# Performance work log

Hardware: AMD Instinct MI355X
Metric: run time of the kernel (lower is better)

The kernel has to match this reference:

```python
import jax, jax.numpy as jnp
from jax import lax
import numpy as np

N = 10                      # spline knots
STEP = 1.0 / (N - 1)
B, E, NC, H, W = 64, 2, 8, 256, 256

def _interp_matrix(n, step):
    # natural-cubic-spline second-derivative solve matrix (constant, numpy at trace time)
    mat = 4.0 * np.eye(n - 2)
    np.fill_diagonal(mat[1:, :-1], 1.0)
    np.fill_diagonal(mat[:-1, 1:], 1.0)
    A = 6.0 * np.linalg.inv(mat) / step ** 2
    z = np.zeros(n - 2)
    A = np.vstack([z, A, z])
    Bm = np.zeros([n - 2, n])
    np.fill_diagonal(Bm, 1.0)
    np.fill_diagonal(Bm[:, 1:], -2.0)
    np.fill_diagonal(Bm[:, 2:], 1.0)
    return (A @ Bm).astype(np.float32)

MAT = jnp.asarray(_interp_matrix(N, STEP))  # (N, N)


def setup_inputs() -> dict:
    key = jax.random.key(0)
    ks = iter(jax.random.split(key, 40))
    def w(shape, scale=0.05):
        return jax.random.normal(next(ks), shape, jnp.float32) * scale
    d = {"batch": jax.random.uniform(next(ks), (B, 3, H, W), jnp.float32)}
    chans = [3, NC, 2 * NC, 4 * NC, 8 * NC, 16 * NC]
    for i in range(1, 6):
        d[f"w{i}"] = w((chans[i], chans[i - 1], 3, 3))
        d[f"bias{i}"] = jnp.zeros((chans[i],), jnp.float32)
    for i in range(2, 6):
        c = chans[i]
        d[f"bn{i}_gamma"] = jnp.ones((c,), jnp.float32)
        d[f"bn{i}_beta"] = jnp.zeros((c,), jnp.float32)
        d[f"bn{i}_mean"] = jnp.zeros((c,), jnp.float32)
        d[f"bn{i}_var"] = jnp.ones((c,), jnp.float32)
    d["l1_w"] = w((16 * NC, 16 * NC))
    d["l1_b"] = jnp.zeros((16 * NC,), jnp.float32)
    d["l2_w"] = w((3 * N * E, 16 * NC))
    d["l2_b"] = jnp.zeros((3 * N * E,), jnp.float32)
    return d


def _conv(x, w, b):
    y = lax.conv_general_dilated(x, w, (2, 2), 'VALID',
                                 dimension_numbers=('NCHW', 'OIHW', 'NCHW'))
    return y + b[None, :, None, None]


def _bn(x, g, beta, m, v):
    s = (g * lax.rsqrt(v + 1e-5))
    return (x - m[None, :, None, None]) * s[None, :, None, None] + beta[None, :, None, None]


def _coeffs(yt):
    # yt: (B, E, 3, N) knot values (ys + identity). Returns a,b,c,d each (B,E,3,N-1).
    M = jnp.einsum('ij,becj->beci', MAT, yt)
    h = STEP
    a = (M[..., 1:] - M[..., :-1]) / (6.0 * h)
    b = M[..., :-1] / 2.0
    c = (yt[..., 1:] - yt[..., :-1]) / h - (M[..., 1:] + 2.0 * M[..., :-1]) * (h / 6.0)
    d = yt[..., :-1]
    return a, b, c, d


def _apply(a, b, c, d, xi, xf):
    # a..d: (B,E,3,N-1); xi int (B,E,3,P); xf float broadcastable to (B,E,3,P)
    ga = jnp.take_along_axis(a, xi, axis=-1)
    gb = jnp.take_along_axis(b, xi, axis=-1)
    gc = jnp.take_along_axis(c, xi, axis=-1)
    gd = jnp.take_along_axis(d, xi, axis=-1)
    return ((ga * xf + gb) * xf + gc) * xf + gd


def reference(batch, w1, bias1, w2, bias2, w3, bias3, w4, bias4, w5, bias5,
              bn2_gamma, bn2_beta, bn2_mean, bn2_var,
              bn3_gamma, bn3_beta, bn3_mean, bn3_var,
              bn4_gamma, bn4_beta, bn4_mean, bn4_var,
              bn5_gamma, bn5_beta, bn5_mean, bn5_var,
              l1_w, l1_b, l2_w, l2_b):
    y = jax.nn.relu(_conv(batch, w1, bias1))
    y = _bn(jax.nn.relu(_conv(y, w2, bias2)), bn2_gamma, bn2_beta, bn2_mean, bn2_var)
    y = _bn(jax.nn.relu(_conv(y, w3, bias3)), bn3_gamma, bn3_beta, bn3_mean, bn3_var)
    y = _bn(jax.nn.relu(_conv(y, w4, bias4)), bn4_gamma, bn4_beta, bn4_mean, bn4_var)
    y = _bn(jax.nn.relu(_conv(y, w5, bias5)), bn5_gamma, bn5_beta, bn5_mean, bn5_var)
    feat = jnp.mean(y, axis=(2, 3))                      # AvgPool2d(7) on 7x7 -> (B, 16*NC)
    hh = jax.nn.relu(feat @ l1_w.T + l1_b)
    ys = (hh @ l2_w.T + l2_b).reshape(B, E, 3, N)        # per-expert per-channel knot residuals
    identity = (jnp.arange(N, dtype=jnp.float32) / (N - 1))
    yt = ys + identity                                   # residual curves around identity
    a, b, c, d = _coeffs(yt)                             # each (B,E,3,N-1)

    # per-pixel bucketize + coefficient gather + cubic Horner eval
    P = H * W
    xv = batch.reshape(B, 3, P)
    xi = jnp.clip(jnp.floor(xv / STEP), 0, N - 2).astype(jnp.int32)
    xf = (xv - xi.astype(jnp.float32) * STEP)[:, None, :, :]       # (B,1,3,P)
    idx = jnp.broadcast_to(xi[:, None, :, :], (B, E, 3, P))
    out = _apply(a, b, c, d, idx, xf)                              # (B,E,3,P)
    out = out.reshape(B, E, 3, H, W).transpose(1, 0, 2, 3, 4)      # (E,B,3,H,W)

    # sampled spline curves over 255 uniform values
    vals = jnp.arange(0.0, 1.0, 1.0 / 255, dtype=jnp.float32)      # (255,)
    V = vals.shape[0]
    vi = jnp.clip(jnp.floor(vals / STEP), 0, N - 2).astype(jnp.int32)
    vf = vals - vi.astype(jnp.float32) * STEP
    vidx = jnp.broadcast_to(vi[None, None, None, :], (B, E, 3, V))
    splines = _apply(a, b, c, d, vidx, vf[None, None, None, :])    # (B,E,3,V)
    splines = splines.transpose(1, 0, 2, 3)                        # (E,B,3,V)
    return out, splines
```

## Files before the change

kernel.cpp:

```cpp
#include <hip/hip_runtime.h>
#include <hip/hip_bf16.h>

#define STEP_F (1.0f/9.0f)

typedef float f4 __attribute__((ext_vector_type(4)));

__global__ __launch_bounds__(256) void conv12_k(
    const float* __restrict__ x,
    const float* __restrict__ w1c, const float* __restrict__ b1c,
    const float* __restrict__ w2c, const float* __restrict__ b2c,
    const float* __restrict__ g, const float* __restrict__ be,
    const float* __restrict__ mn, const float* __restrict__ vr,
    float* __restrict__ y2)
{
    __shared__ float y1t[8 * 1188 + 16];
    const int b    = blockIdx.x;
    const int ohg  = blockIdx.y;
    const int tid  = threadIdx.x;
    const int rows = (127 - 8 * ohg) < 9 ? (127 - 8 * ohg) : 9;

    {
        const int owg = tid & 31;
        const int rg  = tid >> 5;
        const float* xb = x + (size_t)b * 3 * 65536;
        for (int r = rg; r < rows; r += 8) {
            const int r1  = 8 * ohg + r;
            const int ih0 = 2 * r1;
            const int iw0 = owg * 8;
            float acc1[8][4];
            #pragma unroll
            for (int c = 0; c < 8; ++c)
                #pragma unroll
                for (int t = 0; t < 4; ++t) acc1[c][t] = 0.0f;

            #pragma unroll
            for (int ci = 0; ci < 3; ++ci) {
                float rr[3][10];
                #pragma unroll
                for (int kh = 0; kh < 3; ++kh) {
                    const float* row = xb + ci * 65536 + (ih0 + kh) * 256;
                    #pragma unroll
                    for (int t = 0; t < 5; ++t) {
                        int c = iw0 + 2 * t; if (c > 254) c = 254;
                        float2 v = *(const float2*)(row + c);
                        rr[kh][2*t] = v.x; rr[kh][2*t+1] = v.y;
                    }
                }
                #pragma unroll
                for (int co = 0; co < 8; ++co) {
                    float wr[9];
                    #pragma unroll
                    for (int k = 0; k < 9; ++k) wr[k] = w1c[(co * 3 + ci) * 9 + k];
                    #pragma unroll
                    for (int t = 0; t < 4; ++t) {
                        float a = acc1[co][t];
                        #pragma unroll
                        for (int kh = 0; kh < 3; ++kh)
                            a = fmaf(rr[kh][2*t+0], wr[kh*3+0],
                                fmaf(rr[kh][2*t+1], wr[kh*3+1],
                                fmaf(rr[kh][2*t+2], wr[kh*3+2], a)));
                        acc1[co][t] = a;
                    }
                }
            }
            #pragma unroll
            for (int co = 0; co < 8; ++co) {
                float bs = b1c[co];
                f4 o;
                o[0] = fmaxf(acc1[co][0] + bs, 0.0f);
                o[1] = fmaxf(acc1[co][1] + bs, 0.0f);
                o[2] = fmaxf(acc1[co][2] + bs, 0.0f);
                o[3] = fmaxf(acc1[co][3] + bs, 0.0f);
                *(f4*)&y1t[co * 1188 + r * 132 + owg * 4] = o;
            }
        }
    }
    __syncthreads();

    {
        const int lane = tid & 63;
        const int wv   = __builtin_amdgcn_readfirstlane(tid >> 6);
        const int ow   = lane;
        const int co0  = wv * 4;

        float acc[4][4];
        #pragma unroll
        for (int c = 0; c < 4; ++c)
            #pragma unroll
            for (int j = 0; j < 4; ++j) acc[c][j] = 0.0f;

        #pragma unroll 2
        for (int ci = 0; ci < 8; ++ci) {
            float wr[4][9];
            #pragma unroll
            for (int c = 0; c < 4; ++c) {
                const int wb = __builtin_amdgcn_readfirstlane(((co0 + c) * 8 + ci) * 9);
                #pragma unroll
                for (int k = 0; k < 9; ++k) wr[c][k] = w2c[wb + k];
            }
            const float* lci = y1t + ci * 1188;
            #pragma unroll
            for (int r = 0; r < 9; ++r) {
                float2 x01 = *(const float2*)&lci[r * 132 + 2 * ow];
                float  x2  = lci[r * 132 + 2 * ow + 2];
                #pragma unroll
                for (int kh = 0; kh < 3; ++kh) {
                    const int jj = r - kh;
                    if (jj >= 0 && (jj & 1) == 0 && (jj >> 1) < 4) {
                        const int j = jj >> 1;
                        #pragma unroll
                        for (int c = 0; c < 4; ++c)
                            acc[c][j] = fmaf(x01.x, wr[c][kh*3+0],
                                        fmaf(x01.y, wr[c][kh*3+1],
                                        fmaf(x2,    wr[c][kh*3+2], acc[c][j])));
                    }
                }
            }
        }

        if (ow < 63) {
            #pragma unroll
            for (int c = 0; c < 4; ++c) {
                const int co = co0 + c;
                const float bs = b2c[co];
                const float s  = g[co] / sqrtf(vr[co] + 1e-5f);
                const float sh = be[co] - mn[co] * s;
                #pragma unroll
                for (int j = 0; j < 4; ++j) {
                    int oh = 4 * ohg + j;
                    if (oh < 63)
                        y2[(((size_t)b * 16 + co) * 63 + oh) * 64 + ow] =
                            fmaxf(acc[c][j] + bs, 0.0f) * s + sh;
                }
            }
        }
    }
}

__global__ __launch_bounds__(256) void conv3c_k(
    const float* __restrict__ x,
    const float* __restrict__ w, const float* __restrict__ bias,
    const float* __restrict__ g, const float* __restrict__ be,
    const float* __restrict__ mn, const float* __restrict__ vr,
    float* __restrict__ y)
{
    const int b   = blockIdx.x;
    const int ohg = blockIdx.y;
    const int coh = blockIdx.z;
    const int lane = threadIdx.x & 63;
    const int wv   = __builtin_amdgcn_readfirstlane(threadIdx.x >> 6);
    const int ow   = lane & 31;
    const int ohl  = lane >> 5;
    const int co0  = coh * 8 + wv * 2;
    const int ihb  = ohg * 8 + ohl * 4;

    float acc[2][2];
    #pragma unroll
    for (int c = 0; c < 2; ++c) { acc[c][0] = 0.0f; acc[c][1] = 0.0f; }

    #pragma unroll 2
    for (int ci = 0; ci < 16; ++ci) {
        const float* gp = x + (((size_t)b * 16 + ci) * 63) * 64 + 2 * ow;
        f4 rv[5];
        #pragma unroll
        for (int r = 0; r < 5; ++r) {
            int ih = ihb + r; ih = ih > 62 ? 62 : ih;
            rv[r] = *(const f4*)(gp + ih * 64);
        }
        float wr[2][9];
        #pragma unroll
        for (int c = 0; c < 2; ++c) {
            const int wb = __builtin_amdgcn_readfirstlane(((co0 + c) * 16 + ci) * 9);
            #pragma unroll
            for (int k = 0; k < 9; ++k) wr[c][k] = w[wb + k];
        }
        #pragma unroll
        for (int j = 0; j < 2; ++j)
            #pragma unroll
            for (int kh = 0; kh < 3; ++kh) {
                const f4 v = rv[2*j + kh];
                #pragma unroll
                for (int c = 0; c < 2; ++c)
                    acc[c][j] = fmaf(v[0], wr[c][kh*3+0],
                                fmaf(v[1], wr[c][kh*3+1],
                                fmaf(v[2], wr[c][kh*3+2], acc[c][j])));
            }
    }

    if (ow < 31) {
        #pragma unroll
        for (int c = 0; c < 2; ++c) {
            const int co = co0 + c;
            const float bs = bias[co];
            const float s  = g[co] / sqrtf(vr[co] + 1e-5f);
            const float sh = be[co] - mn[co] * s;
            #pragma unroll
            for (int j = 0; j < 2; ++j) {
                int oh = ohg * 4 + ohl * 2 + j;
                if (oh < 31)
                    y[(((size_t)b * 32 + co) * 31 + oh) * 32 + ow] =
                        fmaxf(acc[c][j] + bs, 0.0f) * s + sh;
            }
        }
    }
}

__global__ __launch_bounds__(256) void conv4c_k(
    const float* __restrict__ x,
    const float* __restrict__ w, const float* __restrict__ bias,
    const float* __restrict__ g, const float* __restrict__ be,
    const float* __restrict__ mn, const float* __restrict__ vr,
    float* __restrict__ y)
{
    const int b   = blockIdx.x;
    const int ohg = blockIdx.y;
    const int cog = blockIdx.z;
    const int lane = threadIdx.x & 63;
    const int wv   = __builtin_amdgcn_readfirstlane(threadIdx.x >> 6);
    const int ow   = lane & 15;
    const int ohl  = lane >> 4;
    const int oh   = ohg * 4 + ohl;
    const int co0  = cog * 8 + wv * 2;
    const int ihb  = 2 * oh;

    float acc[2];
    acc[0] = 0.0f; acc[1] = 0.0f;

    #pragma unroll 4
    for (int ci = 0; ci < 32; ++ci) {
        const float* gp = x + (((size_t)b * 32 + ci) * 31) * 32 + 2 * ow;
        f4 rv[3];
        #pragma unroll
        for (int r = 0; r < 3; ++r) {
            int ih = ihb + r; ih = ih > 30 ? 30 : ih;
            rv[r] = *(const f4*)(gp + ih * 32);
        }
        float wr[2][9];
        #pragma unroll
        for (int c = 0; c < 2; ++c) {
            const int wb = __builtin_amdgcn_readfirstlane(((co0 + c) * 32 + ci) * 9);
            #pragma unroll
            for (int k = 0; k < 9; ++k) wr[c][k] = w[wb + k];
        }
        #pragma unroll
        for (int kh = 0; kh < 3; ++kh) {
            const f4 v = rv[kh];
            #pragma unroll
            for (int c = 0; c < 2; ++c)
                acc[c] = fmaf(v[0], wr[c][kh*3+0],
                         fmaf(v[1], wr[c][kh*3+1],
                         fmaf(v[2], wr[c][kh*3+2], acc[c])));
        }
    }

    if (ow < 15 && oh < 15) {
        #pragma unroll
        for (int c = 0; c < 2; ++c) {
            const int co = co0 + c;
            const float bs = bias[co];
            const float s  = g[co] / sqrtf(vr[co] + 1e-5f);
            const float sh = be[co] - mn[co] * s;
            y[(((size_t)b * 64 + co) * 15 + oh) * 16 + ow] =
                fmaxf(acc[c] + bs, 0.0f) * s + sh;
        }
    }
}

__global__ __launch_bounds__(256) void conv5m3_k(
    const float* __restrict__ x,
    const float* __restrict__ w, const float* __restrict__ bias,
    const float* __restrict__ g, const float* __restrict__ be,
    const float* __restrict__ mn, const float* __restrict__ vr,
    float* __restrict__ feat)
{
    __shared__ float red[4 * 325 + 16];
    const int b    = blockIdx.x;
    const int co0  = blockIdx.y * 4;
    const int tid  = threadIdx.x;
    const int wv   = __builtin_amdgcn_readfirstlane(tid >> 6);
    const int lane = tid & 63;
    const int pr = lane >> 3, pc = lane & 7;

    float acc[4];
    #pragma unroll
    for (int c = 0; c < 4; ++c) acc[c] = 0.0f;

    #pragma unroll 4
    for (int i = 0; i < 16; ++i) {
        const int ci = wv * 16 + i;
        const float* gp = x + (((size_t)b * 64 + ci) * 15) * 16 + 2 * pc;
        f4 rv[3];
        #pragma unroll
        for (int r = 0; r < 3; ++r) {
            int ih = 2 * pr + r; ih = ih > 14 ? 14 : ih;
            rv[r] = *(const f4*)(gp + ih * 16);
        }
        float wr[4][9];
        #pragma unroll
        for (int c = 0; c < 4; ++c) {
            const int wb = __builtin_amdgcn_readfirstlane(((co0 + c) * 64 + ci) * 9);
            #pragma unroll
            for (int k = 0; k < 9; ++k) wr[c][k] = w[wb + k];
        }
        #pragma unroll
        for (int kh = 0; kh < 3; ++kh) {
            const f4 v = rv[kh];
            #pragma unroll
            for (int c = 0; c < 4; ++c)
                acc[c] = fmaf(v[0], wr[c][kh*3+0],
                         fmaf(v[1], wr[c][kh*3+1],
                         fmaf(v[2], wr[c][kh*3+2], acc[c])));
        }
    }

    #pragma unroll
    for (int c = 0; c < 4; ++c) red[wv * 325 + lane * 5 + c] = acc[c];
    __syncthreads();
    if (wv == 0) {
        const bool act = (pr < 7) && (pc < 7);
        #pragma unroll
        for (int c = 0; c < 4; ++c) {
            float v = red[lane*5+c] + red[325+lane*5+c]
                    + red[650+lane*5+c] + red[975+lane*5+c];
            const int co = co0 + c;
            const float s = g[co] / sqrtf(vr[co] + 1e-5f);
            v = fmaxf(v + bias[co], 0.0f) * s + (be[co] - mn[co] * s);
            v = act ? v : 0.0f;
            #pragma unroll
            for (int off = 32; off; off >>= 1) v += __shfl_xor(v, off, 64);
            if (lane == 0) feat[(size_t)b * 128 + co] = v * (1.0f / 49.0f);
        }
    }
}

__global__ __launch_bounds__(256) void tail_k(
    const float* __restrict__ featg, const float* __restrict__ l1w,
    const float* __restrict__ l1b, const float* __restrict__ l2w,
    const float* __restrict__ l2b, float* __restrict__ coef,
    float* __restrict__ spl)
{
    __shared__ float feat[128];
    __shared__ float hh[128];
    __shared__ float ysv[64];
    __shared__ float cfl[216];
    const int b = blockIdx.x, t = threadIdx.x;

    if (t < 128) feat[t] = featg[(size_t)b * 128 + t];
    __syncthreads();
    if (t < 128) {
        const float4* wp = (const float4*)(l1w + (size_t)t * 128);
        float s = l1b[t];
        #pragma unroll 8
        for (int k = 0; k < 32; ++k) {
            float4 v = wp[k];
            s += v.x*feat[4*k] + v.y*feat[4*k+1] + v.z*feat[4*k+2] + v.w*feat[4*k+3];
        }
        hh[t] = fmaxf(s, 0.0f);
    }
    __syncthreads();
    if (t < 60) {
        const float4* wp = (const float4*)(l2w + (size_t)t * 128);
        float s = l2b[t];
        #pragma unroll 8
        for (int k = 0; k < 32; ++k) {
            float4 v = wp[k];
            s += v.x*hh[4*k] + v.y*hh[4*k+1] + v.z*hh[4*k+2] + v.w*hh[4*k+3];
        }
        ysv[t] = s;
    }
    __syncthreads();
    if (t < 6) {
        const float h = STEP_F;
        float yt[10];
        #pragma unroll
        for (int n = 0; n < 10; ++n) yt[n] = ysv[t * 10 + n] + (float)n * h;
        float r[8];
        const float k6h2 = 6.0f / (h * h);
        #pragma unroll
        for (int i = 0; i < 8; ++i) r[i] = k6h2 * (yt[i] - 2.0f * yt[i+1] + yt[i+2]);
        float cp[8], dp[8];
        cp[0] = 0.25f; dp[0] = r[0] * 0.25f;
        #pragma unroll
        for (int i = 1; i < 8; ++i) {
            float m = 4.0f - cp[i-1];
            cp[i] = 1.0f / m;
            dp[i] = (r[i] - dp[i-1]) / m;
        }
        float M[10];
        M[0] = 0.0f; M[9] = 0.0f; M[8] = dp[7];
        #pragma unroll
        for (int i = 6; i >= 0; --i) M[i+1] = dp[i] - cp[i] * M[i+2];
        float* cg = coef + ((size_t)b * 6 + t) * 36;
        #pragma unroll
        for (int i = 0; i < 9; ++i) {
            float ca = (M[i+1] - M[i]) / (6.0f * h);
            float cb = M[i] * 0.5f;
            float cc = (yt[i+1] - yt[i]) / h - (M[i+1] + 2.0f * M[i]) * (h / 6.0f);
            float cd = yt[i];
            cfl[t*36 + i]      = ca;  cg[i]      = ca;
            cfl[t*36 + 9 + i]  = cb;  cg[9 + i]  = cb;
            cfl[t*36 + 18 + i] = cc;  cg[18 + i] = cc;
            cfl[t*36 + 27 + i] = cd;  cg[27 + i] = cd;
        }
    }
    __syncthreads();
    for (int i = t; i < 1530; i += 256) {
        int v = i % 255, ec = i / 255;
        float val = (float)v * (1.0f / 255.0f);
        int vi = (int)floorf(val / STEP_F);
        vi = vi < 0 ? 0 : (vi > 8 ? 8 : vi);
        float vf = val - (float)vi * STEP_F;
        const float* c = cfl + ec * 36;
        int e = ec / 3, ch = ec % 3;
        spl[(((size_t)e * 64 + b) * 3 + ch) * 255 + v] =
            ((c[vi]*vf + c[9+vi])*vf + c[18+vi])*vf + c[27+vi];
    }
}

__global__ __launch_bounds__(256) void apply2_k(const float* __restrict__ batch,
                                                const float* __restrict__ coef,
                                                float* __restrict__ out)
{
    int bc = blockIdx.y;
    int b = bc / 3, ch = bc % 3;
    int lane = threadIdx.x & 63;
    int j = lane < 9 ? lane : 8;
    const float* c0p = coef + ((size_t)(b * 6 + 0 + ch)) * 36;
    const float* c1p = coef + ((size_t)(b * 6 + 3 + ch)) * 36;
    float A0 = c0p[j], B0 = c0p[9 + j], C0 = c0p[18 + j], D0 = c0p[27 + j];
    float A1 = c1p[j], B1 = c1p[9 + j], C1 = c1p[18 + j], D1 = c1p[27 + j];

    const int P = 65536;
    size_t base = ((size_t)b * 3 + ch) * P;
    int p0 = (blockIdx.x * blockDim.x + threadIdx.x) * 4;

    float4 xv = *(const float4*)(batch + base + p0);
    float xs[4] = {xv.x, xv.y, xv.z, xv.w};
    float r0[4], r1[4];
    #pragma unroll
    for (int k = 0; k < 4; ++k) {
        float x = xs[k];
        int xi = (int)floorf(x / STEP_F);
        xi = xi < 0 ? 0 : (xi > 8 ? 8 : xi);
        float xf = x - (float)xi * STEP_F;
        int bidx = xi << 2;
        float ga0 = __int_as_float(__builtin_amdgcn_ds_bpermute(bidx, __float_as_int(A0)));
        float gb0 = __int_as_float(__builtin_amdgcn_ds_bpermute(bidx, __float_as_int(B0)));
        float gc0 = __int_as_float(__builtin_amdgcn_ds_bpermute(bidx, __float_as_int(C0)));
        float gd0 = __int_as_float(__builtin_amdgcn_ds_bpermute(bidx, __float_as_int(D0)));
        float ga1 = __int_as_float(__builtin_amdgcn_ds_bpermute(bidx, __float_as_int(A1)));
        float gb1 = __int_as_float(__builtin_amdgcn_ds_bpermute(bidx, __float_as_int(B1)));
        float gc1 = __int_as_float(__builtin_amdgcn_ds_bpermute(bidx, __float_as_int(C1)));
        float gd1 = __int_as_float(__builtin_amdgcn_ds_bpermute(bidx, __float_as_int(D1)));
        r0[k] = fmaf(fmaf(fmaf(ga0, xf, gb0), xf, gc0), xf, gd0);
        r1[k] = fmaf(fmaf(fmaf(ga1, xf, gb1), xf, gc1), xf, gd1);
    }
    float4 o0 = {r0[0], r0[1], r0[2], r0[3]};
    float4 o1 = {r1[0], r1[1], r1[2], r1[3]};
    size_t off0 = (((size_t)0 * 64 + b) * 3 + ch) * P + p0;
    size_t off1 = (((size_t)1 * 64 + b) * 3 + ch) * P + p0;
    *(float4*)(out + off0) = o0;
    *(float4*)(out + off1) = o1;
}

extern "C" void kernel_launch(void* const* d_in, const int* in_sizes, int n_in,
                              void* d_out, int out_size, void* d_ws, size_t ws_size,
                              hipStream_t stream) {
    const float* batch = (const float*)d_in[0];
    const float* w1 = (const float*)d_in[1];  const float* b1 = (const float*)d_in[2];
    const float* w2 = (const float*)d_in[3];  const float* b2 = (const float*)d_in[4];
    const float* w3 = (const float*)d_in[5];  const float* b3 = (const float*)d_in[6];
    const float* w4 = (const float*)d_in[7];  const float* b4 = (const float*)d_in[8];
    const float* w5 = (const float*)d_in[9];  const float* b5 = (const float*)d_in[10];
    const float* bn2g = (const float*)d_in[11]; const float* bn2b = (const float*)d_in[12];
    const float* bn2m = (const float*)d_in[13]; const float* bn2v = (const float*)d_in[14];
    const float* bn3g = (const float*)d_in[15]; const float* bn3b = (const float*)d_in[16];
    const float* bn3m = (const float*)d_in[17]; const float* bn3v = (const float*)d_in[18];
    const float* bn4g = (const float*)d_in[19]; const float* bn4b = (const float*)d_in[20];
    const float* bn4m = (const float*)d_in[21]; const float* bn4v = (const float*)d_in[22];
    const float* bn5g = (const float*)d_in[23]; const float* bn5b = (const float*)d_in[24];
    const float* bn5m = (const float*)d_in[25]; const float* bn5v = (const float*)d_in[26];
    const float* l1w = (const float*)d_in[27]; const float* l1b = (const float*)d_in[28];
    const float* l2w = (const float*)d_in[29]; const float* l2b = (const float*)d_in[30];

    float* outp = (float*)d_out;
    float* y2 = outp;
    float* y3 = y2 + 4128768;
    float* y4 = y3 + 2031616;

    float* coef  = (float*)d_ws;
    float* featw = coef + 13824;

    const int TPB = 256;
    conv12_k<<<dim3(64, 16), TPB, 0, stream>>>(batch, w1, b1, w2, b2,
                                               bn2g, bn2b, bn2m, bn2v, y2);
    conv3c_k<<<dim3(64, 8, 4), TPB, 0, stream>>>(y2, w3, b3, bn3g, bn3b, bn3m, bn3v, y3);
    conv4c_k<<<dim3(64, 4, 8), TPB, 0, stream>>>(y3, w4, b4, bn4g, bn4b, bn4m, bn4v, y4);
    conv5m3_k<<<dim3(64, 32), TPB, 0, stream>>>(y4, w5, b5, bn5g, bn5b, bn5m, bn5v, featw);
    tail_k<<<64, TPB, 0, stream>>>(featw, l1w, l1b, l2w, l2b, coef, outp + 25165824);
    {
        dim3 grid(64, 192);
        apply2_k<<<grid, TPB, 0, stream>>>(batch, coef, outp);
    }
}
```

Before: 145.5 us.

## Widen conv channel tiles, stage conv5 weights in LDS, fuse tail into apply

conv3 and conv4 now compute four output channels per wave instead of two, halving their grids so each input load feeds more FMAs. conv5 computes eight channels per block and stages the block's weight slice in shared memory instead of issuing scalar global loads. The separate tail kernel (MLP plus spline coefficients) is folded into the apply kernel, so each block recomputes the MLP for its (batch, channel) and then loops over eight pixel chunks; this drops one launch and the coefficient round-trip through workspace. In exchange the MLP is computed redundantly in every block, there is less parallelism in the convs, and register pressure rises.

```diff
diff --git a/kernel.cpp b/kernel.cpp
--- a/kernel.cpp
+++ b/kernel.cpp
@@ -137,7 +137,7 @@
     }
 }
 
-__global__ __launch_bounds__(256) void conv3c_k(
+__global__ __launch_bounds__(256) void conv3_k(
     const float* __restrict__ x,
     const float* __restrict__ w, const float* __restrict__ bias,
     const float* __restrict__ g, const float* __restrict__ be,
@@ -151,14 +151,14 @@
     const int wv   = __builtin_amdgcn_readfirstlane(threadIdx.x >> 6);
     const int ow   = lane & 31;
     const int ohl  = lane >> 5;
-    const int co0  = coh * 8 + wv * 2;
+    const int co0  = coh * 16 + wv * 4;
     const int ihb  = ohg * 8 + ohl * 4;
 
-    float acc[2][2];
+    float acc[4][2];
     #pragma unroll
-    for (int c = 0; c < 2; ++c) { acc[c][0] = 0.0f; acc[c][1] = 0.0f; }
-
-    #pragma unroll 2
+    for (int c = 0; c < 4; ++c) { acc[c][0] = 0.0f; acc[c][1] = 0.0f; }
+
+    #pragma unroll 4
     for (int ci = 0; ci < 16; ++ci) {
         const float* gp = x + (((size_t)b * 16 + ci) * 63) * 64 + 2 * ow;
         f4 rv[5];
@@ -167,9 +167,9 @@
             int ih = ihb + r; ih = ih > 62 ? 62 : ih;
             rv[r] = *(const f4*)(gp + ih * 64);
         }
-        float wr[2][9];
-        #pragma unroll
-        for (int c = 0; c < 2; ++c) {
+        float wr[4][9];
+        #pragma unroll
+        for (int c = 0; c < 4; ++c) {
             const int wb = __builtin_amdgcn_readfirstlane(((co0 + c) * 16 + ci) * 9);
             #pragma unroll
             for (int k = 0; k < 9; ++k) wr[c][k] = w[wb + k];
@@ -180,7 +180,7 @@
             for (int kh = 0; kh < 3; ++kh) {
                 const f4 v = rv[2*j + kh];
                 #pragma unroll
-                for (int c = 0; c < 2; ++c)
+                for (int c = 0; c < 4; ++c)
                     acc[c][j] = fmaf(v[0], wr[c][kh*3+0],
                                 fmaf(v[1], wr[c][kh*3+1],
                                 fmaf(v[2], wr[c][kh*3+2], acc[c][j])));
@@ -189,7 +189,7 @@
 
     if (ow < 31) {
         #pragma unroll
-        for (int c = 0; c < 2; ++c) {
+        for (int c = 0; c < 4; ++c) {
             const int co = co0 + c;
             const float bs = bias[co];
             const float s  = g[co] / sqrtf(vr[co] + 1e-5f);
@@ -205,7 +205,7 @@
     }
 }
 
-__global__ __launch_bounds__(256) void conv4c_k(
+__global__ __launch_bounds__(256) void conv4_k(
     const float* __restrict__ x,
     const float* __restrict__ w, const float* __restrict__ bias,
     const float* __restrict__ g, const float* __restrict__ be,
@@ -220,11 +220,12 @@
     const int ow   = lane & 15;
     const int ohl  = lane >> 4;
     const int oh   = ohg * 4 + ohl;
-    const int co0  = cog * 8 + wv * 2;
+    const int co0  = cog * 16 + wv * 4;
     const int ihb  = 2 * oh;
 
-    float acc[2];
-    acc[0] = 0.0f; acc[1] = 0.0f;
+    float acc[4];
+    #pragma unroll
+    for (int c = 0; c < 4; ++c) acc[c] = 0.0f;
 
     #pragma unroll 4
     for (int ci = 0; ci < 32; ++ci) {
@@ -235,9 +236,9 @@
             int ih = ihb + r; ih = ih > 30 ? 30 : ih;
             rv[r] = *(const f4*)(gp + ih * 32);
         }
-        float wr[2][9];
-        #pragma unroll
-        for (int c = 0; c < 2; ++c) {
+        float wr[4][9];
+        #pragma unroll
+        for (int c = 0; c < 4; ++c) {
             const int wb = __builtin_amdgcn_readfirstlane(((co0 + c) * 32 + ci) * 9);
             #pragma unroll
             for (int k = 0; k < 9; ++k) wr[c][k] = w[wb + k];
@@ -246,7 +247,7 @@
         for (int kh = 0; kh < 3; ++kh) {
             const f4 v = rv[kh];
             #pragma unroll
-            for (int c = 0; c < 2; ++c)
+            for (int c = 0; c < 4; ++c)
                 acc[c] = fmaf(v[0], wr[c][kh*3+0],
                          fmaf(v[1], wr[c][kh*3+1],
                          fmaf(v[2], wr[c][kh*3+2], acc[c])));
@@ -255,7 +256,7 @@
 
     if (ow < 15 && oh < 15) {
         #pragma unroll
-        for (int c = 0; c < 2; ++c) {
+        for (int c = 0; c < 4; ++c) {
             const int co = co0 + c;
             const float bs = bias[co];
             const float s  = g[co] / sqrtf(vr[co] + 1e-5f);
@@ -266,26 +267,34 @@
     }
 }
 
-__global__ __launch_bounds__(256) void conv5m3_k(
+__global__ __launch_bounds__(256) void conv5w_k(
     const float* __restrict__ x,
     const float* __restrict__ w, const float* __restrict__ bias,
     const float* __restrict__ g, const float* __restrict__ be,
     const float* __restrict__ mn, const float* __restrict__ vr,
     float* __restrict__ feat)
 {
-    __shared__ float red[4 * 325 + 16];
+    __shared__ float lw[4608];
+    __shared__ float red[4 * 580 + 16];
     const int b    = blockIdx.x;
-    const int co0  = blockIdx.y * 4;
+    const int co0  = blockIdx.y * 8;
     const int tid  = threadIdx.x;
+
+    {
+        const float* wp = w + (size_t)co0 * 576;
+        for (int i = tid; i < 4608; i += 256) lw[i] = wp[i];
+    }
+    __syncthreads();
+
     const int wv   = __builtin_amdgcn_readfirstlane(tid >> 6);
     const int lane = tid & 63;
     const int pr = lane >> 3, pc = lane & 7;
 
-    float acc[4];
+    float acc[8];
     #pragma unroll
-    for (int c = 0; c < 4; ++c) acc[c] = 0.0f;
-
-    #pragma unroll 4
+    for (int c = 0; c < 8; ++c) acc[c] = 0.0f;
+
+    #pragma unroll 2
     for (int i = 0; i < 16; ++i) {
         const int ci = wv * 16 + i;
         const float* gp = x + (((size_t)b * 64 + ci) * 15) * 16 + 2 * pc;
@@ -295,18 +304,18 @@
             int ih = 2 * pr + r; ih = ih > 14 ? 14 : ih;
             rv[r] = *(const f4*)(gp + ih * 16);
         }
-        float wr[4][9];
-        #pragma unroll
-        for (int c = 0; c < 4; ++c) {
-            const int wb = __builtin_amdgcn_readfirstlane(((co0 + c) * 64 + ci) * 9);
-            #pragma unroll
-            for (int k = 0; k < 9; ++k) wr[c][k] = w[wb + k];
+        float wr[8][9];
+        #pragma unroll
+        for (int c = 0; c < 8; ++c) {
+            const float* lwp = lw + (c * 64 + ci) * 9;
+            #pragma unroll
+            for (int k = 0; k < 9; ++k) wr[c][k] = lwp[k];
         }
         #pragma unroll
         for (int kh = 0; kh < 3; ++kh) {
             const f4 v = rv[kh];
             #pragma unroll
-            for (int c = 0; c < 4; ++c)
+            for (int c = 0; c < 8; ++c)
                 acc[c] = fmaf(v[0], wr[c][kh*3+0],
                          fmaf(v[1], wr[c][kh*3+1],
                          fmaf(v[2], wr[c][kh*3+2], acc[c])));
@@ -314,14 +323,14 @@
     }
 
     #pragma unroll
-    for (int c = 0; c < 4; ++c) red[wv * 325 + lane * 5 + c] = acc[c];
+    for (int c = 0; c < 8; ++c) red[wv * 580 + lane * 9 + c] = acc[c];
     __syncthreads();
     if (wv == 0) {
         const bool act = (pr < 7) && (pc < 7);
         #pragma unroll
-        for (int c = 0; c < 4; ++c) {
-            float v = red[lane*5+c] + red[325+lane*5+c]
-                    + red[650+lane*5+c] + red[975+lane*5+c];
+        for (int c = 0; c < 8; ++c) {
+            float v = red[lane*9+c] + red[580+lane*9+c]
+                    + red[1160+lane*9+c] + red[1740+lane*9+c];
             const int co = co0 + c;
             const float s = g[co] / sqrtf(vr[co] + 1e-5f);
             v = fmaxf(v + bias[co], 0.0f) * s + (be[co] - mn[co] * s);
@@ -333,17 +342,19 @@
     }
 }
 
-__global__ __launch_bounds__(256) void tail_k(
-    const float* __restrict__ featg, const float* __restrict__ l1w,
-    const float* __restrict__ l1b, const float* __restrict__ l2w,
-    const float* __restrict__ l2b, float* __restrict__ coef,
-    float* __restrict__ spl)
+__global__ __launch_bounds__(256) void applyT_k(
+    const float* __restrict__ batch, const float* __restrict__ featg,
+    const float* __restrict__ l1w, const float* __restrict__ l1b,
+    const float* __restrict__ l2w, const float* __restrict__ l2b,
+    float* __restrict__ out, float* __restrict__ spl)
 {
     __shared__ float feat[128];
     __shared__ float hh[128];
-    __shared__ float ysv[64];
-    __shared__ float cfl[216];
-    const int b = blockIdx.x, t = threadIdx.x;
+    __shared__ float ysv[20];
+    __shared__ float cfl[72];
+    const int bc = blockIdx.y;
+    const int b = bc / 3, ch = bc % 3;
+    const int t = threadIdx.x;
 
     if (t < 128) feat[t] = featg[(size_t)b * 128 + t];
     __syncthreads();
@@ -358,9 +369,11 @@
         hh[t] = fmaxf(s, 0.0f);
     }
     __syncthreads();
-    if (t < 60) {
-        const float4* wp = (const float4*)(l2w + (size_t)t * 128);
-        float s = l2b[t];
+    if (t < 20) {
+        const int e = t / 10, n = t % 10;
+        const int row = e * 30 + ch * 10 + n;
+        const float4* wp = (const float4*)(l2w + (size_t)row * 128);
+        float s = l2b[row];
         #pragma unroll 8
         for (int k = 0; k < 32; ++k) {
             float4 v = wp[k];
@@ -369,7 +382,7 @@
         ysv[t] = s;
     }
     __syncthreads();
-    if (t < 6) {
+    if (t < 2) {
         const float h = STEP_F;
         float yt[10];
         #pragma unroll
@@ -390,77 +403,66 @@
         M[0] = 0.0f; M[9] = 0.0f; M[8] = dp[7];
         #pragma unroll
         for (int i = 6; i >= 0; --i) M[i+1] = dp[i] - cp[i] * M[i+2];
-        float* cg = coef + ((size_t)b * 6 + t) * 36;
+        float* cf = cfl + t * 36;
         #pragma unroll
         for (int i = 0; i < 9; ++i) {
-            float ca = (M[i+1] - M[i]) / (6.0f * h);
-            float cb = M[i] * 0.5f;
-            float cc = (yt[i+1] - yt[i]) / h - (M[i+1] + 2.0f * M[i]) * (h / 6.0f);
-            float cd = yt[i];
-            cfl[t*36 + i]      = ca;  cg[i]      = ca;
-            cfl[t*36 + 9 + i]  = cb;  cg[9 + i]  = cb;
-            cfl[t*36 + 18 + i] = cc;  cg[18 + i] = cc;
-            cfl[t*36 + 27 + i] = cd;  cg[27 + i] = cd;
-        }
-    }
-    __syncthreads();
-    for (int i = t; i < 1530; i += 256) {
-        int v = i % 255, ec = i / 255;
-        float val = (float)v * (1.0f / 255.0f);
-        int vi = (int)floorf(val / STEP_F);
-        vi = vi < 0 ? 0 : (vi > 8 ? 8 : vi);
-        float vf = val - (float)vi * STEP_F;
-        const float* c = cfl + ec * 36;
-        int e = ec / 3, ch = ec % 3;
-        spl[(((size_t)e * 64 + b) * 3 + ch) * 255 + v] =
-            ((c[vi]*vf + c[9+vi])*vf + c[18+vi])*vf + c[27+vi];
-    }
-}
-
-__global__ __launch_bounds__(256) void apply2_k(const float* __restrict__ batch,
-                                                const float* __restrict__ coef,
-                                                float* __restrict__ out)
-{
-    int bc = blockIdx.y;
-    int b = bc / 3, ch = bc % 3;
-    int lane = threadIdx.x & 63;
-    int j = lane < 9 ? lane : 8;
-    const float* c0p = coef + ((size_t)(b * 6 + 0 + ch)) * 36;
-    const float* c1p = coef + ((size_t)(b * 6 + 3 + ch)) * 36;
-    float A0 = c0p[j], B0 = c0p[9 + j], C0 = c0p[18 + j], D0 = c0p[27 + j];
-    float A1 = c1p[j], B1 = c1p[9 + j], C1 = c1p[18 + j], D1 = c1p[27 + j];
+            cf[i]      = (M[i+1] - M[i]) / (6.0f * h);
+            cf[9 + i]  = M[i] * 0.5f;
+            cf[18 + i] = (yt[i+1] - yt[i]) / h - (M[i+1] + 2.0f * M[i]) * (h / 6.0f);
+            cf[27 + i] = yt[i];
+        }
+    }
+    __syncthreads();
+
+    const int lane = t & 63;
+    const int j = lane < 9 ? lane : 8;
+    const float A0 = cfl[j],      B0 = cfl[9 + j],  C0 = cfl[18 + j], D0 = cfl[27 + j];
+    const float A1 = cfl[36 + j], B1 = cfl[45 + j], C1 = cfl[54 + j], D1 = cfl[63 + j];
 
     const int P = 65536;
-    size_t base = ((size_t)b * 3 + ch) * P;
-    int p0 = (blockIdx.x * blockDim.x + threadIdx.x) * 4;
-
-    float4 xv = *(const float4*)(batch + base + p0);
-    float xs[4] = {xv.x, xv.y, xv.z, xv.w};
-    float r0[4], r1[4];
-    #pragma unroll
-    for (int k = 0; k < 4; ++k) {
-        float x = xs[k];
-        int xi = (int)floorf(x / STEP_F);
-        xi = xi < 0 ? 0 : (xi > 8 ? 8 : xi);
-        float xf = x - (float)xi * STEP_F;
-        int bidx = xi << 2;
-        float ga0 = __int_as_float(__builtin_amdgcn_ds_bpermute(bidx, __float_as_int(A0)));
-        float gb0 = __int_as_float(__builtin_amdgcn_ds_bpermute(bidx, __float_as_int(B0)));
-        float gc0 = __int_as_float(__builtin_amdgcn_ds_bpermute(bidx, __float_as_int(C0)));
-        float gd0 = __int_as_float(__builtin_amdgcn_ds_bpermute(bidx, __float_as_int(D0)));
-        float ga1 = __int_as_float(__builtin_amdgcn_ds_bpermute(bidx, __float_as_int(A1)));
-        float gb1 = __int_as_float(__builtin_amdgcn_ds_bpermute(bidx, __float_as_int(B1)));
-        float gc1 = __int_as_float(__builtin_amdgcn_ds_bpermute(bidx, __float_as_int(C1)));
-        float gd1 = __int_as_float(__builtin_amdgcn_ds_bpermute(bidx, __float_as_int(D1)));
-        r0[k] = fmaf(fmaf(fmaf(ga0, xf, gb0), xf, gc0), xf, gd0);
-        r1[k] = fmaf(fmaf(fmaf(ga1, xf, gb1), xf, gc1), xf, gd1);
-    }
-    float4 o0 = {r0[0], r0[1], r0[2], r0[3]};
-    float4 o1 = {r1[0], r1[1], r1[2], r1[3]};
-    size_t off0 = (((size_t)0 * 64 + b) * 3 + ch) * P + p0;
-    size_t off1 = (((size_t)1 * 64 + b) * 3 + ch) * P + p0;
-    *(float4*)(out + off0) = o0;
-    *(float4*)(out + off1) = o1;
+    const size_t base = ((size_t)b * 3 + ch) * P;
+    #pragma unroll 1
+    for (int it = 0; it < 8; ++it) {
+        const int p0 = ((blockIdx.x * 8 + it) * 256 + t) * 4;
+        float4 xv = *(const float4*)(batch + base + p0);
+        float xs[4] = {xv.x, xv.y, xv.z, xv.w};
+        float r0[4], r1[4];
+        #pragma unroll
+        for (int k = 0; k < 4; ++k) {
+            float x = xs[k];
+            int xi = (int)floorf(x / STEP_F);
+            xi = xi < 0 ? 0 : (xi > 8 ? 8 : xi);
+            float xf = x - (float)xi * STEP_F;
+            int bidx = xi << 2;
+            float ga0 = __int_as_float(__builtin_amdgcn_ds_bpermute(bidx, __float_as_int(A0)));
+            float gb0 = __int_as_float(__builtin_amdgcn_ds_bpermute(bidx, __float_as_int(B0)));
+            float gc0 = __int_as_float(__builtin_amdgcn_ds_bpermute(bidx, __float_as_int(C0)));
+            float gd0 = __int_as_float(__builtin_amdgcn_ds_bpermute(bidx, __float_as_int(D0)));
+            float ga1 = __int_as_float(__builtin_amdgcn_ds_bpermute(bidx, __float_as_int(A1)));
+            float gb1 = __int_as_float(__builtin_amdgcn_ds_bpermute(bidx, __float_as_int(B1)));
+            float gc1 = __int_as_float(__builtin_amdgcn_ds_bpermute(bidx, __float_as_int(C1)));
+            float gd1 = __int_as_float(__builtin_amdgcn_ds_bpermute(bidx, __float_as_int(D1)));
+            r0[k] = fmaf(fmaf(fmaf(ga0, xf, gb0), xf, gc0), xf, gd0);
+            r1[k] = fmaf(fmaf(fmaf(ga1, xf, gb1), xf, gc1), xf, gd1);
+        }
+        float4 o0 = {r0[0], r0[1], r0[2], r0[3]};
+        float4 o1 = {r1[0], r1[1], r1[2], r1[3]};
+        *(float4*)(out + (((size_t)0 * 64 + b) * 3 + ch) * P + p0) = o0;
+        *(float4*)(out + (((size_t)1 * 64 + b) * 3 + ch) * P + p0) = o1;
+    }
+
+    if (blockIdx.x == 0) {
+        for (int i = t; i < 510; i += 256) {
+            const int e = i / 255, v = i % 255;
+            float val = (float)v * (1.0f / 255.0f);
+            int vi = (int)floorf(val / STEP_F);
+            vi = vi < 0 ? 0 : (vi > 8 ? 8 : vi);
+            float vf = val - (float)vi * STEP_F;
+            const float* c = cfl + e * 36;
+            spl[(((size_t)e * 64 + b) * 3 + ch) * 255 + v] =
+                ((c[vi]*vf + c[9+vi])*vf + c[18+vi])*vf + c[27+vi];
+        }
+    }
 }
 
 extern "C" void kernel_launch(void* const* d_in, const int* in_sizes, int n_in,
@@ -488,18 +490,15 @@
     float* y3 = y2 + 4128768;
     float* y4 = y3 + 2031616;
 
-    float* coef  = (float*)d_ws;
-    float* featw = coef + 13824;
+    float* featw = (float*)d_ws;
+    float* spl   = outp + 25165824;
 
     const int TPB = 256;
     conv12_k<<<dim3(64, 16), TPB, 0, stream>>>(batch, w1, b1, w2, b2,
                                                bn2g, bn2b, bn2m, bn2v, y2);
-    conv3c_k<<<dim3(64, 8, 4), TPB, 0, stream>>>(y2, w3, b3, bn3g, bn3b, bn3m, bn3v, y3);
-    conv4c_k<<<dim3(64, 4, 8), TPB, 0, stream>>>(y3, w4, b4, bn4g, bn4b, bn4m, bn4v, y4);
-    conv5m3_k<<<dim3(64, 32), TPB, 0, stream>>>(y4, w5, b5, bn5g, bn5b, bn5m, bn5v, featw);
-    tail_k<<<64, TPB, 0, stream>>>(featw, l1w, l1b, l2w, l2b, coef, outp + 25165824);
-    {
-        dim3 grid(64, 192);
-        apply2_k<<<grid, TPB, 0, stream>>>(batch, coef, outp);
-    }
+    conv3_k<<<dim3(64, 8, 2), TPB, 0, stream>>>(y2, w3, b3, bn3g, bn3b, bn3m, bn3v, y3);
+    conv4_k<<<dim3(64, 4, 4), TPB, 0, stream>>>(y3, w4, b4, bn4g, bn4b, bn4m, bn4v, y4);
+    conv5w_k<<<dim3(64, 16), TPB, 0, stream>>>(y4, w5, b5, bn5g, bn5b, bn5m, bn5v, featw);
+    applyT_k<<<dim3(8, 192), TPB, 0, stream>>>(batch, featw, l1w, l1b, l2w, l2b,
+                                               outp, spl);
 }
```

After: 140.3 us. -3.5%, faster.
